# Kernel tuning notes

Measured on AMD Instinct MI355X. Metric: run time of the kernel, lower is better.

The kernel has to match this reference:

```python
import jax, jax.numpy as jnp
import numpy as np

PUPIL = 256          # pupil / OPD grid size
OUTPUT_DIM = 64      # cropped PSF postage-stamp size
N_BINS = 8           # number of SED wavelength bins
BATCH = 16
# Static, wavelength-dependent diffraction padding sizes (phase_N per bin).
# In the original these come from packed_SED_data[:,0,:] but are constant in a FoV.
PHASE_NS = [1024, 988, 952, 918, 886, 856, 828, 802]


def setup_inputs() -> dict:
    key = jax.random.key(0)
    k1, k2, k3 = jax.random.split(key, 3)
    # OPD in meters: small wavefront errors (~lambda/10 rms)
    opd_batch = jax.random.normal(k1, (BATCH, PUPIL, PUPIL), dtype=jnp.float32) * 1e-7
    # Annular pupil: outer aperture with central obscuration (like Euclid/VIS optics)
    yy, xx = np.mgrid[:PUPIL, :PUPIL].astype(np.float32)
    c = (PUPIL - 1) / 2.0
    r = np.sqrt((xx - c) ** 2 + (yy - c) ** 2) / (PUPIL / 2.0)
    obscurations = jnp.asarray(((r <= 1.0) & (r >= 0.3)).astype(np.float32))
    # Observed wavelengths per bin, in meters (visible band)
    lambdas = jnp.linspace(0.55e-6, 0.9e-6, N_BINS).astype(jnp.float32)
    # Normalized SED weights
    sed = jax.random.uniform(k2, (N_BINS,), dtype=jnp.float32) + 0.1
    sed_norms = sed / jnp.sum(sed)
    return {
        "opd_batch": opd_batch,
        "obscurations": obscurations,
        "lambdas": lambdas,
        "sed_norms": sed_norms,
    }


def _mono_psf(opd, obsc, lam, phase_N, out_dim):
    """Batched monochromatic PSF: OPD -> phase -> padded FFT -> cropped |.|^2, unit-sum."""
    # opd: [B, p, p]; phase = exp(i * 2pi/lambda * opd) * obscurations
    pre_phase = (2.0 * jnp.pi / lam) * opd
    phase = (jnp.cos(pre_phase) + 1j * jnp.sin(pre_phase)).astype(jnp.complex64)
    phase = phase * obsc.astype(jnp.complex64)
    p = opd.shape[-1]
    pad_lo = (phase_N - p) // 2
    pad_hi = phase_N - p - pad_lo
    padded = jnp.pad(phase, ((0, 0), (pad_lo, pad_hi), (pad_lo, pad_hi)))  # [B, N, N]
    fft = jnp.fft.fftshift(jnp.fft.fft2(padded), axes=(-2, -1))
    psf = fft.real ** 2 + fft.imag ** 2  # |FFT|^2, float32
    start = phase_N // 2 - out_dim // 2
    psf = psf[:, start:start + out_dim, start:start + out_dim]  # central crop
    return psf / jnp.sum(psf, axis=(-2, -1), keepdims=True)


def reference(opd_batch, obscurations, lambdas, sed_norms):
    # Polychromatic PSF: SED-weighted sum of monochromatic PSFs over wavelength bins.
    # Loop is over the small fixed set of bins (distinct static FFT sizes);
    # each bin is fully vectorized over the batch.
    out = jnp.zeros((opd_batch.shape[0], OUTPUT_DIM, OUTPUT_DIM), dtype=jnp.float32)
    for b, phase_N in enumerate(PHASE_NS):
        out = out + sed_norms[b] * _mono_psf(
            opd_batch, obscurations, lambdas[b], phase_N, OUTPUT_DIM
        )
    return out
```

## Files before the change

kernel.cpp:

```cpp
#include <hip/hip_runtime.h>
#include <math.h>

#define PUPIL 256
#define N_BINS 8
#define BATCH 16

__constant__ int PHASE_NS_C[N_BINS] = {1024, 988, 952, 918, 886, 856, 828, 802};

typedef short bf16x8 __attribute__((ext_vector_type(8)));
typedef short bf16x4 __attribute__((ext_vector_type(4)));
typedef float f32x4  __attribute__((ext_vector_type(4)));
typedef int   i32x4  __attribute__((ext_vector_type(4)));

#define MFMA16(a, b, c) __builtin_amdgcn_mfma_f32_16x16x32_bf16((a), (b), (c), 0, 0, 0)

__device__ __forceinline__ short f2bf(float f) {
  unsigned u = __float_as_uint(f);
  u += 0x7FFFu + ((u >> 16) & 1u);
  return (short)(u >> 16);
}
__device__ __forceinline__ bf16x8 neg8(bf16x8 v) {
  i32x4 t = __builtin_bit_cast(i32x4, v);
  t ^= (int)0x80008000;
  return __builtin_bit_cast(bf16x8, t);
}


__global__ void wprep(short* __restrict__ Wr_t, short* __restrict__ Wi_t) {
  int idx = blockIdx.x * 256 + threadIdx.x;
  int n   = idx & 255;
  int k   = (idx >> 8) & 63;
  int bin = idx >> 14;
  int N = PHASE_NS_C[bin];
  int m = ((k - 32) * n) % N;
  if (m < 0) m += N;
  float ang = -6.283185307179586f * (float)m / (float)N;
  float s, c;
  __sincosf(ang, &s, &c);
  Wr_t[idx] = f2bf(c);
  Wi_t[idx] = f2bf(s);
}

__global__ __launch_bounds__(256, 4) void stage1(
    const float* __restrict__ opd, const float* __restrict__ obsc,
    const float* __restrict__ lambdas,
    const short* __restrict__ Wr_t, const short* __restrict__ Wi_t,
    short* __restrict__ Gr_t, short* __restrict__ Gi_t)
{
  const int tid = threadIdx.x;
  const int yb = blockIdx.x * 32, bin = blockIdx.y, b = blockIdx.z;
  const int bb = b * N_BINS + bin;
  const float w0 = 6.283185307179586f / lambdas[bin];

  __shared__ short Pr[32 * 32], Pi[32 * 32];

  const int wave = tid >> 6, lane = tid & 63;
  const int lr = lane & 15, lq = lane >> 4;

  f32x4 aR[2], aI[2];
  aR[0] = (f32x4)0.0f; aR[1] = (f32x4)0.0f;
  aI[0] = (f32x4)0.0f; aI[1] = (f32x4)0.0f;

  const int gy = tid >> 3;
  const int gx = (tid & 7) * 4;
  const float* orow = opd + ((size_t)b * PUPIL + yb + gy) * PUPIL;
  const float* brow = obsc + (size_t)(yb + gy) * PUPIL;
  const short* wrb = Wr_t + ((size_t)bin * 64 + wave * 16 + lr) * 256 + lq * 8;
  const short* wib = Wi_t + ((size_t)bin * 64 + wave * 16 + lr) * 256 + lq * 8;

  for (int xc = 0; xc < 8; ++xc) {
    const int xb = xc * 32;
    const float4 od = *(const float4*)(orow + xb + gx);
    const float4 ob = *(const float4*)(brow + xb + gx);
    bf16x4 vr, vi;
    {
      float s, c;
      __sincosf(w0 * od.x, &s, &c); vr[0] = f2bf(c * ob.x); vi[0] = f2bf(s * ob.x);
      __sincosf(w0 * od.y, &s, &c); vr[1] = f2bf(c * ob.y); vi[1] = f2bf(s * ob.y);
      __sincosf(w0 * od.z, &s, &c); vr[2] = f2bf(c * ob.z); vi[2] = f2bf(s * ob.z);
      __sincosf(w0 * od.w, &s, &c); vr[3] = f2bf(c * ob.w); vi[3] = f2bf(s * ob.w);
    }
    __syncthreads();
    *(bf16x4*)&Pr[gy * 32 + gx] = vr;
    *(bf16x4*)&Pi[gy * 32 + gx] = vi;
    const bf16x8 w_r  = *(const bf16x8*)(wrb + xb);
    const bf16x8 w_i  = *(const bf16x8*)(wib + xb);
    const bf16x8 nw_i = neg8(w_i);
    __syncthreads();

    for (int t = 0; t < 2; ++t) {
      const bf16x8 pr = *(const bf16x8*)&Pr[(t * 16 + lr) * 32 + lq * 8];
      const bf16x8 pi = *(const bf16x8*)&Pi[(t * 16 + lr) * 32 + lq * 8];
      aR[t] = MFMA16(w_r,  pr, aR[t]);
      aR[t] = MFMA16(nw_i, pi, aR[t]);
      aI[t] = MFMA16(w_r,  pi, aI[t]);
      aI[t] = MFMA16(w_i,  pr, aI[t]);
    }
  }

  #pragma unroll
  for (int t = 0; t < 2; ++t) {
    const int y = yb + t * 16 + lr;
    #pragma unroll
    for (int r = 0; r < 4; ++r) {
      const int kv = wave * 16 + lq * 4 + r;
      const size_t o = ((size_t)bb * 64 + kv) * 256 + y;
      Gr_t[o] = f2bf(aR[t][r]);
      Gi_t[o] = f2bf(aI[t][r]);
    }
  }
}

__global__ __launch_bounds__(256, 4) void stage2(
    const short* __restrict__ Wr_t, const short* __restrict__ Wi_t,
    const short* __restrict__ Gr_t, const short* __restrict__ Gi_t,
    float* __restrict__ psf_raw, float* __restrict__ sums)
{
  const int tid = threadIdx.x;
  const int uc = blockIdx.x, bin = blockIdx.y, b = blockIdx.z;
  const int bb = b * N_BINS + bin;

  __shared__ float pvbuf[64 * 17];
  __shared__ float red[4];

  const int wave = tid >> 6, lane = tid & 63;
  const int lr = lane & 15, lq = lane >> 4;

  f32x4 hR = (f32x4)0.0f, hI = (f32x4)0.0f;

  const short* grb = Gr_t + ((size_t)bb * 64 + wave * 16 + lr) * 256 + lq * 8;
  const short* gib = Gi_t + ((size_t)bb * 64 + wave * 16 + lr) * 256 + lq * 8;
  const short* wrb = Wr_t + ((size_t)bin * 64 + uc * 16 + lr) * 256 + lq * 8;
  const short* wib = Wi_t + ((size_t)bin * 64 + uc * 16 + lr) * 256 + lq * 8;

  for (int yc = 0; yc < 8; ++yc) {
    const int yb = yc * 32;
    const bf16x8 g_r  = *(const bf16x8*)(grb + yb);
    const bf16x8 g_i  = *(const bf16x8*)(gib + yb);
    const bf16x8 w_r  = *(const bf16x8*)(wrb + yb);
    const bf16x8 w_i  = *(const bf16x8*)(wib + yb);
    const bf16x8 ng_i = neg8(g_i);
    hR = MFMA16(g_r,  w_r, hR);
    hR = MFMA16(ng_i, w_i, hR);
    hI = MFMA16(g_r,  w_i, hI);
    hI = MFMA16(g_i,  w_r, hI);
  }

  float pv[4], lsum = 0.f;
  #pragma unroll
  for (int r = 0; r < 4; ++r) {
    pv[r] = hR[r] * hR[r] + hI[r] * hI[r];
    lsum += pv[r];
  }
  #pragma unroll
  for (int off = 32; off > 0; off >>= 1) lsum += __shfl_down(lsum, off);
  if (lane == 0) red[wave] = lsum;

  #pragma unroll
  for (int r = 0; r < 4; ++r)
    pvbuf[(wave * 16 + lq * 4 + r) * 17 + lr] = pv[r];
  __syncthreads();

  if (tid == 0)
    sums[bb * 4 + uc] = red[0] + red[1] + red[2] + red[3];

  #pragma unroll
  for (int it = 0; it < 4; ++it) {
    const int i  = tid + it * 256;
    const int ul = i >> 6;
    const int v  = i & 63;
    psf_raw[(size_t)bb * 4096 + (uc * 16 + ul) * 64 + v] = pvbuf[v * 17 + ul];
  }
}

__global__ void combine(const float* __restrict__ psf_raw,
                        const float* __restrict__ sums,
                        const float* __restrict__ sed,
                        float* __restrict__ out) {
  __shared__ float sc[N_BINS];
  const int blk = blockIdx.x;
  const int b = blk >> 4;
  const int px = (blk & 15) * 256 + threadIdx.x;
  if (threadIdx.x < N_BINS) {
    const int bb = b * N_BINS + threadIdx.x;
    const float S = sums[bb * 4] + sums[bb * 4 + 1] + sums[bb * 4 + 2] + sums[bb * 4 + 3];
    sc[threadIdx.x] = sed[threadIdx.x] / S;
  }
  __syncthreads();
  float acc = 0.f;
  #pragma unroll
  for (int bin = 0; bin < N_BINS; ++bin)
    acc += sc[bin] * psf_raw[(size_t)(b * N_BINS + bin) * 4096 + px];
  out[b * 4096 + px] = acc;
}

extern "C" void kernel_launch(void* const* d_in, const int* in_sizes, int n_in,
                              void* d_out, int out_size, void* d_ws, size_t ws_size,
                              hipStream_t stream) {
  const float* opd     = (const float*)d_in[0];
  const float* obsc    = (const float*)d_in[1];
  const float* lambdas = (const float*)d_in[2];
  const float* sed     = (const float*)d_in[3];
  float* out = (float*)d_out;

  short* Wr_t = (short*)d_ws;
  short* Wi_t = Wr_t + (size_t)N_BINS * 64 * 256;
  short* Gr_t = Wi_t + (size_t)N_BINS * 64 * 256;
  short* Gi_t = Gr_t + (size_t)BATCH * N_BINS * 64 * 256;
  float* psf_raw = (float*)(Gi_t + (size_t)BATCH * N_BINS * 64 * 256);
  float* sums    = psf_raw + (size_t)BATCH * N_BINS * 4096;

  wprep<<<512, 256, 0, stream>>>(Wr_t, Wi_t);
  stage1<<<dim3(8, N_BINS, BATCH), 256, 0, stream>>>(opd, obsc, lambdas,
                                                     Wr_t, Wi_t, Gr_t, Gi_t);
  stage2<<<dim3(4, N_BINS, BATCH), 256, 0, stream>>>(Wr_t, Wi_t, Gr_t, Gi_t,
                                                     psf_raw, sums);
  combine<<<256, 256, 0, stream>>>(psf_raw, sums, sed, out);
}
```

Baseline: 88.18 us.

## Fuse twiddle prep into stage1 and combine into stage2 via atomics

Removes the separate twiddle-generation kernel by computing DFT twiddles inline in stage1 with sincos, with one block group per bin also writing them to workspace for stage2. Stage2 now computes the whole 64x64 output per (batch,bin) in one block, normalizes locally, and atomically accumulates SED-weighted results into the output, which stage1 zeroes first. This drops two kernel launches and the psf_raw round trip. In exchange it adds per-block sincos work, atomic float additions whose summation order is nondeterministic, and stage2 runs 4x fewer blocks.

```diff
diff --git a/kernel.cpp b/kernel.cpp
--- a/kernel.cpp
+++ b/kernel.cpp
@@ -26,36 +26,32 @@
 }
 
 
-__global__ void wprep(short* __restrict__ Wr_t, short* __restrict__ Wi_t) {
-  int idx = blockIdx.x * 256 + threadIdx.x;
-  int n   = idx & 255;
-  int k   = (idx >> 8) & 63;
-  int bin = idx >> 14;
-  int N = PHASE_NS_C[bin];
-  int m = ((k - 32) * n) % N;
-  if (m < 0) m += N;
-  float ang = -6.283185307179586f * (float)m / (float)N;
-  float s, c;
-  __sincosf(ang, &s, &c);
-  Wr_t[idx] = f2bf(c);
-  Wi_t[idx] = f2bf(s);
-}
-
 __global__ __launch_bounds__(256, 4) void stage1(
     const float* __restrict__ opd, const float* __restrict__ obsc,
     const float* __restrict__ lambdas,
-    const short* __restrict__ Wr_t, const short* __restrict__ Wi_t,
-    short* __restrict__ Gr_t, short* __restrict__ Gi_t)
+    short* __restrict__ Wr_t, short* __restrict__ Wi_t,
+    short* __restrict__ Gr_t, short* __restrict__ Gi_t,
+    float* __restrict__ out)
 {
   const int tid = threadIdx.x;
   const int yb = blockIdx.x * 32, bin = blockIdx.y, b = blockIdx.z;
   const int bb = b * N_BINS + bin;
   const float w0 = 6.283185307179586f / lambdas[bin];
+  const int   N  = PHASE_NS_C[bin];
+  const float npiN = -6.283185307179586f / (float)N;
+  const bool  storeW = (blockIdx.z == 0) && (blockIdx.x == 0);
 
   __shared__ short Pr[32 * 32], Pi[32 * 32];
+
+  if (tid < 64) {
+    const int blin = blockIdx.x + 8 * (blockIdx.y + 8 * blockIdx.z);
+    out[blin * 64 + tid] = 0.0f;
+  }
 
   const int wave = tid >> 6, lane = tid & 63;
   const int lr = lane & 15, lq = lane >> 4;
+  const int kv = wave * 16 + lr;
+  const int kvm = kv - 32;
 
   f32x4 aR[2], aI[2];
   aR[0] = (f32x4)0.0f; aR[1] = (f32x4)0.0f;
@@ -65,8 +61,6 @@
   const int gx = (tid & 7) * 4;
   const float* orow = opd + ((size_t)b * PUPIL + yb + gy) * PUPIL;
   const float* brow = obsc + (size_t)(yb + gy) * PUPIL;
-  const short* wrb = Wr_t + ((size_t)bin * 64 + wave * 16 + lr) * 256 + lq * 8;
-  const short* wib = Wi_t + ((size_t)bin * 64 + wave * 16 + lr) * 256 + lq * 8;
 
   for (int xc = 0; xc < 8; ++xc) {
     const int xb = xc * 32;
@@ -80,12 +74,25 @@
       __sincosf(w0 * od.z, &s, &c); vr[2] = f2bf(c * ob.z); vi[2] = f2bf(s * ob.z);
       __sincosf(w0 * od.w, &s, &c); vr[3] = f2bf(c * ob.w); vi[3] = f2bf(s * ob.w);
     }
+    bf16x8 w_r, w_i;
+    {
+      const int x0 = xb + lq * 8;
+      #pragma unroll
+      for (int j = 0; j < 8; ++j) {
+        float s, c;
+        __sincosf((float)(kvm * (x0 + j)) * npiN, &s, &c);
+        w_r[j] = f2bf(c);
+        w_i[j] = f2bf(s);
+      }
+    }
+    const bf16x8 nw_i = neg8(w_i);
+    if (storeW) {
+      *(bf16x8*)&Wr_t[((size_t)bin * 64 + kv) * 256 + xb + lq * 8] = w_r;
+      *(bf16x8*)&Wi_t[((size_t)bin * 64 + kv) * 256 + xb + lq * 8] = w_i;
+    }
     __syncthreads();
     *(bf16x4*)&Pr[gy * 32 + gx] = vr;
     *(bf16x4*)&Pi[gy * 32 + gx] = vi;
-    const bf16x8 w_r  = *(const bf16x8*)(wrb + xb);
-    const bf16x8 w_i  = *(const bf16x8*)(wib + xb);
-    const bf16x8 nw_i = neg8(w_i);
     __syncthreads();
 
     for (int t = 0; t < 2; ++t) {
@@ -103,95 +110,76 @@
     const int y = yb + t * 16 + lr;
     #pragma unroll
     for (int r = 0; r < 4; ++r) {
-      const int kv = wave * 16 + lq * 4 + r;
-      const size_t o = ((size_t)bb * 64 + kv) * 256 + y;
+      const int kvd = wave * 16 + lq * 4 + r;
+      const size_t o = ((size_t)bb * 64 + kvd) * 256 + y;
       Gr_t[o] = f2bf(aR[t][r]);
       Gi_t[o] = f2bf(aI[t][r]);
     }
   }
 }
 
-__global__ __launch_bounds__(256, 4) void stage2(
+__global__ __launch_bounds__(256, 2) void stage2(
     const short* __restrict__ Wr_t, const short* __restrict__ Wi_t,
     const short* __restrict__ Gr_t, const short* __restrict__ Gi_t,
-    float* __restrict__ psf_raw, float* __restrict__ sums)
+    const float* __restrict__ sed, float* __restrict__ out)
 {
   const int tid = threadIdx.x;
-  const int uc = blockIdx.x, bin = blockIdx.y, b = blockIdx.z;
+  const int bin = blockIdx.x, b = blockIdx.y;
   const int bb = b * N_BINS + bin;
 
-  __shared__ float pvbuf[64 * 17];
   __shared__ float red[4];
 
   const int wave = tid >> 6, lane = tid & 63;
   const int lr = lane & 15, lq = lane >> 4;
 
-  f32x4 hR = (f32x4)0.0f, hI = (f32x4)0.0f;
+  f32x4 hR[4], hI[4];
+  #pragma unroll
+  for (int n = 0; n < 4; ++n) { hR[n] = (f32x4)0.0f; hI[n] = (f32x4)0.0f; }
 
   const short* grb = Gr_t + ((size_t)bb * 64 + wave * 16 + lr) * 256 + lq * 8;
   const short* gib = Gi_t + ((size_t)bb * 64 + wave * 16 + lr) * 256 + lq * 8;
-  const short* wrb = Wr_t + ((size_t)bin * 64 + uc * 16 + lr) * 256 + lq * 8;
-  const short* wib = Wi_t + ((size_t)bin * 64 + uc * 16 + lr) * 256 + lq * 8;
+  const size_t wbase = ((size_t)bin * 64 + lr) * 256 + lq * 8;
 
   for (int yc = 0; yc < 8; ++yc) {
     const int yb = yc * 32;
     const bf16x8 g_r  = *(const bf16x8*)(grb + yb);
     const bf16x8 g_i  = *(const bf16x8*)(gib + yb);
-    const bf16x8 w_r  = *(const bf16x8*)(wrb + yb);
-    const bf16x8 w_i  = *(const bf16x8*)(wib + yb);
     const bf16x8 ng_i = neg8(g_i);
-    hR = MFMA16(g_r,  w_r, hR);
-    hR = MFMA16(ng_i, w_i, hR);
-    hI = MFMA16(g_r,  w_i, hI);
-    hI = MFMA16(g_i,  w_r, hI);
-  }
-
-  float pv[4], lsum = 0.f;
-  #pragma unroll
-  for (int r = 0; r < 4; ++r) {
-    pv[r] = hR[r] * hR[r] + hI[r] * hI[r];
-    lsum += pv[r];
-  }
+    for (int n = 0; n < 4; ++n) {
+      const bf16x8 w_r = *(const bf16x8*)(Wr_t + wbase + (size_t)n * 16 * 256 + yb);
+      const bf16x8 w_i = *(const bf16x8*)(Wi_t + wbase + (size_t)n * 16 * 256 + yb);
+      hR[n] = MFMA16(g_r,  w_r, hR[n]);
+      hR[n] = MFMA16(ng_i, w_i, hR[n]);
+      hI[n] = MFMA16(g_r,  w_i, hI[n]);
+      hI[n] = MFMA16(g_i,  w_r, hI[n]);
+    }
+  }
+
+  float pv[4][4], lsum = 0.f;
+  #pragma unroll
+  for (int n = 0; n < 4; ++n)
+    #pragma unroll
+    for (int r = 0; r < 4; ++r) {
+      pv[n][r] = hR[n][r] * hR[n][r] + hI[n][r] * hI[n][r];
+      lsum += pv[n][r];
+    }
   #pragma unroll
   for (int off = 32; off > 0; off >>= 1) lsum += __shfl_down(lsum, off);
   if (lane == 0) red[wave] = lsum;
-
-  #pragma unroll
-  for (int r = 0; r < 4; ++r)
-    pvbuf[(wave * 16 + lq * 4 + r) * 17 + lr] = pv[r];
   __syncthreads();
-
-  if (tid == 0)
-    sums[bb * 4 + uc] = red[0] + red[1] + red[2] + red[3];
-
-  #pragma unroll
-  for (int it = 0; it < 4; ++it) {
-    const int i  = tid + it * 256;
-    const int ul = i >> 6;
-    const int v  = i & 63;
-    psf_raw[(size_t)bb * 4096 + (uc * 16 + ul) * 64 + v] = pvbuf[v * 17 + ul];
-  }
-}
-
-__global__ void combine(const float* __restrict__ psf_raw,
-                        const float* __restrict__ sums,
-                        const float* __restrict__ sed,
-                        float* __restrict__ out) {
-  __shared__ float sc[N_BINS];
-  const int blk = blockIdx.x;
-  const int b = blk >> 4;
-  const int px = (blk & 15) * 256 + threadIdx.x;
-  if (threadIdx.x < N_BINS) {
-    const int bb = b * N_BINS + threadIdx.x;
-    const float S = sums[bb * 4] + sums[bb * 4 + 1] + sums[bb * 4 + 2] + sums[bb * 4 + 3];
-    sc[threadIdx.x] = sed[threadIdx.x] / S;
-  }
-  __syncthreads();
-  float acc = 0.f;
-  #pragma unroll
-  for (int bin = 0; bin < N_BINS; ++bin)
-    acc += sc[bin] * psf_raw[(size_t)(b * N_BINS + bin) * 4096 + px];
-  out[b * 4096 + px] = acc;
+  const float S = red[0] + red[1] + red[2] + red[3];
+  const float scale = sed[bin] / S;
+
+  float* ob = out + (size_t)b * 4096;
+  #pragma unroll
+  for (int n = 0; n < 4; ++n) {
+    const int u = n * 16 + lr;
+    #pragma unroll
+    for (int r = 0; r < 4; ++r) {
+      const int v = wave * 16 + lq * 4 + r;
+      atomicAdd(&ob[u * 64 + v], pv[n][r] * scale);
+    }
+  }
 }
 
 extern "C" void kernel_launch(void* const* d_in, const int* in_sizes, int n_in,
@@ -207,13 +195,9 @@
   short* Wi_t = Wr_t + (size_t)N_BINS * 64 * 256;
   short* Gr_t = Wi_t + (size_t)N_BINS * 64 * 256;
   short* Gi_t = Gr_t + (size_t)BATCH * N_BINS * 64 * 256;
-  float* psf_raw = (float*)(Gi_t + (size_t)BATCH * N_BINS * 64 * 256);
-  float* sums    = psf_raw + (size_t)BATCH * N_BINS * 4096;
-
-  wprep<<<512, 256, 0, stream>>>(Wr_t, Wi_t);
+
   stage1<<<dim3(8, N_BINS, BATCH), 256, 0, stream>>>(opd, obsc, lambdas,
-                                                     Wr_t, Wi_t, Gr_t, Gi_t);
-  stage2<<<dim3(4, N_BINS, BATCH), 256, 0, stream>>>(Wr_t, Wi_t, Gr_t, Gi_t,
-                                                     psf_raw, sums);
-  combine<<<256, 256, 0, stream>>>(psf_raw, sums, sed, out);
-}
+                                                     Wr_t, Wi_t, Gr_t, Gi_t, out);
+  stage2<<<dim3(N_BINS, BATCH), 256, 0, stream>>>(Wr_t, Wi_t, Gr_t, Gi_t,
+                                                  sed, out);
+}
```

New measurement: 97.22 us. +10.2%, slower.

## Fuse all stages into one cooperative kernel with grid syncs and in-register twiddles

Applied to the files above, without the earlier changes.

Merges the twiddle-prep, both DFT matmul stages and the SED combine into a single cooperative kernel of 256 blocks of 512 threads, separated by grid-wide syncs. This removes three kernel launches and the gaps between them. Stage-1 twiddles are now generated in registers by angle-recurrence rotation instead of being loaded from global memory. Blocks with b==0 and yc==0 also write the twiddles out for stage 2 to read. The trade-offs are grid-sync overhead, the need for every block to be co-resident, and some bf16 accuracy drift from the recurrence.

```diff
diff --git a/kernel.cpp b/kernel.cpp
--- a/kernel.cpp
+++ b/kernel.cpp
@@ -1,5 +1,8 @@
 #include <hip/hip_runtime.h>
+#include <hip/hip_cooperative_groups.h>
 #include <math.h>
+
+namespace cg = cooperative_groups;
 
 #define PUPIL 256
 #define N_BINS 8
@@ -26,172 +29,182 @@
 }
 
 
-__global__ void wprep(short* __restrict__ Wr_t, short* __restrict__ Wi_t) {
-  int idx = blockIdx.x * 256 + threadIdx.x;
-  int n   = idx & 255;
-  int k   = (idx >> 8) & 63;
-  int bin = idx >> 14;
-  int N = PHASE_NS_C[bin];
-  int m = ((k - 32) * n) % N;
-  if (m < 0) m += N;
-  float ang = -6.283185307179586f * (float)m / (float)N;
-  float s, c;
-  __sincosf(ang, &s, &c);
-  Wr_t[idx] = f2bf(c);
-  Wi_t[idx] = f2bf(s);
-}
-
-__global__ __launch_bounds__(256, 4) void stage1(
+__global__ __launch_bounds__(512, 2) void mega(
     const float* __restrict__ opd, const float* __restrict__ obsc,
-    const float* __restrict__ lambdas,
-    const short* __restrict__ Wr_t, const short* __restrict__ Wi_t,
-    short* __restrict__ Gr_t, short* __restrict__ Gi_t)
+    const float* __restrict__ lambdas, const float* __restrict__ sed,
+    short* __restrict__ Wr_t, short* __restrict__ Wi_t,
+    short* __restrict__ Gr_t, short* __restrict__ Gi_t,
+    float* __restrict__ psf_raw, float* __restrict__ sums,
+    float* __restrict__ out)
 {
+  const int blk = blockIdx.x;
   const int tid = threadIdx.x;
-  const int yb = blockIdx.x * 32, bin = blockIdx.y, b = blockIdx.z;
-  const int bb = b * N_BINS + bin;
-  const float w0 = 6.283185307179586f / lambdas[bin];
-
-  __shared__ short Pr[32 * 32], Pi[32 * 32];
-
-  const int wave = tid >> 6, lane = tid & 63;
+  const int h    = tid >> 8;
+  const int htid = tid & 255;
+
+  __shared__ short Pr[2][32 * 32], Pi[2][32 * 32];
+  __shared__ float pvbuf[2][64 * 17];
+  __shared__ float red[2][4];
+  __shared__ float sc[N_BINS];
+
+  const int wave = htid >> 6, lane = htid & 63;
   const int lr = lane & 15, lq = lane >> 4;
 
-  f32x4 aR[2], aI[2];
-  aR[0] = (f32x4)0.0f; aR[1] = (f32x4)0.0f;
-  aI[0] = (f32x4)0.0f; aI[1] = (f32x4)0.0f;
-
-  const int gy = tid >> 3;
-  const int gx = (tid & 7) * 4;
-  const float* orow = opd + ((size_t)b * PUPIL + yb + gy) * PUPIL;
-  const float* brow = obsc + (size_t)(yb + gy) * PUPIL;
-  const short* wrb = Wr_t + ((size_t)bin * 64 + wave * 16 + lr) * 256 + lq * 8;
-  const short* wib = Wi_t + ((size_t)bin * 64 + wave * 16 + lr) * 256 + lq * 8;
-
-  for (int xc = 0; xc < 8; ++xc) {
-    const int xb = xc * 32;
-    const float4 od = *(const float4*)(orow + xb + gx);
-    const float4 ob = *(const float4*)(brow + xb + gx);
-    bf16x4 vr, vi;
-    {
-      float s, c;
-      __sincosf(w0 * od.x, &s, &c); vr[0] = f2bf(c * ob.x); vi[0] = f2bf(s * ob.x);
-      __sincosf(w0 * od.y, &s, &c); vr[1] = f2bf(c * ob.y); vi[1] = f2bf(s * ob.y);
-      __sincosf(w0 * od.z, &s, &c); vr[2] = f2bf(c * ob.z); vi[2] = f2bf(s * ob.z);
-      __sincosf(w0 * od.w, &s, &c); vr[3] = f2bf(c * ob.w); vi[3] = f2bf(s * ob.w);
-    }
+  for (int it = 0; it < 2; ++it) {
+    const int unit = (blk * 2 + h) * 2 + it;
+    const int yc = unit & 7, bin = (unit >> 3) & 7, b = unit >> 6;
+    const int yb = yc * 32;
+    const int bb = b * N_BINS + bin;
+    const float w0 = 6.283185307179586f / lambdas[bin];
+    const float npiN = -6.283185307179586f / (float)PHASE_NS_C[bin];
+    const bool storeW = (yc == 0) && (b == 0);
+
+    const int kvm = wave * 16 + lr - 32;
+    float stepS, stepC;
+    __sincosf((float)kvm * npiN, &stepS, &stepC);
+
+    f32x4 aR[2], aI[2];
+    aR[0] = (f32x4)0.0f; aR[1] = (f32x4)0.0f;
+    aI[0] = (f32x4)0.0f; aI[1] = (f32x4)0.0f;
+
+    const int gy = htid >> 3;
+    const int gx = (htid & 7) * 4;
+    const float* orow = opd + ((size_t)b * PUPIL + yb + gy) * PUPIL;
+    const float* brow = obsc + (size_t)(yb + gy) * PUPIL;
+
+    for (int xc = 0; xc < 8; ++xc) {
+      const int xb = xc * 32;
+      const float4 od = *(const float4*)(orow + xb + gx);
+      const float4 ob = *(const float4*)(brow + xb + gx);
+      bf16x4 vr, vi;
+      {
+        float s, c;
+        __sincosf(w0 * od.x, &s, &c); vr[0] = f2bf(c * ob.x); vi[0] = f2bf(s * ob.x);
+        __sincosf(w0 * od.y, &s, &c); vr[1] = f2bf(c * ob.y); vi[1] = f2bf(s * ob.y);
+        __sincosf(w0 * od.z, &s, &c); vr[2] = f2bf(c * ob.z); vi[2] = f2bf(s * ob.z);
+        __sincosf(w0 * od.w, &s, &c); vr[3] = f2bf(c * ob.w); vi[3] = f2bf(s * ob.w);
+      }
+      bf16x8 w_r, w_i;
+      {
+        const int x0 = xb + lq * 8;
+        float ps, pc;
+        __sincosf((float)(kvm * x0) * npiN, &ps, &pc);
+        w_r[0] = f2bf(pc); w_i[0] = f2bf(ps);
+        #pragma unroll
+        for (int j = 1; j < 8; ++j) {
+          const float nc = pc * stepC - ps * stepS;
+          const float ns = pc * stepS + ps * stepC;
+          w_r[j] = f2bf(nc); w_i[j] = f2bf(ns);
+          pc = nc; ps = ns;
+        }
+      }
+      const bf16x8 nw_i = neg8(w_i);
+      if (storeW) {
+        const int kv = wave * 16 + lr;
+        *(bf16x8*)&Wr_t[((size_t)bin * 64 + kv) * 256 + xb + lq * 8] = w_r;
+        *(bf16x8*)&Wi_t[((size_t)bin * 64 + kv) * 256 + xb + lq * 8] = w_i;
+      }
+      __syncthreads();
+      *(bf16x4*)&Pr[h][gy * 32 + gx] = vr;
+      *(bf16x4*)&Pi[h][gy * 32 + gx] = vi;
+      __syncthreads();
+
+      for (int t = 0; t < 2; ++t) {
+        const bf16x8 pr = *(const bf16x8*)&Pr[h][(t * 16 + lr) * 32 + lq * 8];
+        const bf16x8 pi = *(const bf16x8*)&Pi[h][(t * 16 + lr) * 32 + lq * 8];
+        aR[t] = MFMA16(w_r,  pr, aR[t]);
+        aR[t] = MFMA16(nw_i, pi, aR[t]);
+        aI[t] = MFMA16(w_r,  pi, aI[t]);
+        aI[t] = MFMA16(w_i,  pr, aI[t]);
+      }
+    }
+
+    #pragma unroll
+    for (int t = 0; t < 2; ++t) {
+      const int y = yb + t * 16 + lr;
+      #pragma unroll
+      for (int r = 0; r < 4; ++r) {
+        const int kvd = wave * 16 + lq * 4 + r;
+        const size_t o = ((size_t)bb * 64 + kvd) * 256 + y;
+        Gr_t[o] = f2bf(aR[t][r]);
+        Gi_t[o] = f2bf(aI[t][r]);
+      }
+    }
+  }
+
+  cg::this_grid().sync();
+
+  {
+    const int unit = blk * 2 + h;
+    const int uc = unit & 3, bin = (unit >> 2) & 7, b = unit >> 5;
+    const int bb = b * N_BINS + bin;
+
+    f32x4 hR = (f32x4)0.0f, hI = (f32x4)0.0f;
+
+    const short* grb = Gr_t + ((size_t)bb * 64 + wave * 16 + lr) * 256 + lq * 8;
+    const short* gib = Gi_t + ((size_t)bb * 64 + wave * 16 + lr) * 256 + lq * 8;
+    const short* wrb = Wr_t + ((size_t)bin * 64 + uc * 16 + lr) * 256 + lq * 8;
+    const short* wib = Wi_t + ((size_t)bin * 64 + uc * 16 + lr) * 256 + lq * 8;
+
+    for (int yc2 = 0; yc2 < 8; ++yc2) {
+      const int yb2 = yc2 * 32;
+      const bf16x8 g_r  = *(const bf16x8*)(grb + yb2);
+      const bf16x8 g_i  = *(const bf16x8*)(gib + yb2);
+      const bf16x8 w_r  = *(const bf16x8*)(wrb + yb2);
+      const bf16x8 w_i  = *(const bf16x8*)(wib + yb2);
+      const bf16x8 ng_i = neg8(g_i);
+      hR = MFMA16(g_r,  w_r, hR);
+      hR = MFMA16(ng_i, w_i, hR);
+      hI = MFMA16(g_r,  w_i, hI);
+      hI = MFMA16(g_i,  w_r, hI);
+    }
+
+    float pv[4], lsum = 0.f;
+    #pragma unroll
+    for (int r = 0; r < 4; ++r) {
+      pv[r] = hR[r] * hR[r] + hI[r] * hI[r];
+      lsum += pv[r];
+    }
+    #pragma unroll
+    for (int off = 32; off > 0; off >>= 1) lsum += __shfl_down(lsum, off);
+    if (lane == 0) red[h][wave] = lsum;
+
+    #pragma unroll
+    for (int r = 0; r < 4; ++r)
+      pvbuf[h][(wave * 16 + lq * 4 + r) * 17 + lr] = pv[r];
     __syncthreads();
-    *(bf16x4*)&Pr[gy * 32 + gx] = vr;
-    *(bf16x4*)&Pi[gy * 32 + gx] = vi;
-    const bf16x8 w_r  = *(const bf16x8*)(wrb + xb);
-    const bf16x8 w_i  = *(const bf16x8*)(wib + xb);
-    const bf16x8 nw_i = neg8(w_i);
+
+    if (htid == 0)
+      sums[bb * 4 + uc] = red[h][0] + red[h][1] + red[h][2] + red[h][3];
+
+    #pragma unroll
+    for (int it = 0; it < 4; ++it) {
+      const int i  = htid + it * 256;
+      const int ul = i >> 6;
+      const int v  = i & 63;
+      psf_raw[(size_t)bb * 4096 + (uc * 16 + ul) * 64 + v] = pvbuf[h][v * 17 + ul];
+    }
+  }
+
+  cg::this_grid().sync();
+
+  {
+    const int b = blk >> 4;
+    if (tid < N_BINS) {
+      const int bb = b * N_BINS + tid;
+      const float S = sums[bb * 4] + sums[bb * 4 + 1] + sums[bb * 4 + 2] + sums[bb * 4 + 3];
+      sc[tid] = sed[tid] / S;
+    }
     __syncthreads();
-
-    for (int t = 0; t < 2; ++t) {
-      const bf16x8 pr = *(const bf16x8*)&Pr[(t * 16 + lr) * 32 + lq * 8];
-      const bf16x8 pi = *(const bf16x8*)&Pi[(t * 16 + lr) * 32 + lq * 8];
-      aR[t] = MFMA16(w_r,  pr, aR[t]);
-      aR[t] = MFMA16(nw_i, pi, aR[t]);
-      aI[t] = MFMA16(w_r,  pi, aI[t]);
-      aI[t] = MFMA16(w_i,  pr, aI[t]);
+    if (tid < 256) {
+      const int px = (blk & 15) * 256 + tid;
+      float acc = 0.f;
+      #pragma unroll
+      for (int bin = 0; bin < N_BINS; ++bin)
+        acc += sc[bin] * psf_raw[(size_t)(b * N_BINS + bin) * 4096 + px];
+      out[b * 4096 + px] = acc;
     }
   }
-
-  #pragma unroll
-  for (int t = 0; t < 2; ++t) {
-    const int y = yb + t * 16 + lr;
-    #pragma unroll
-    for (int r = 0; r < 4; ++r) {
-      const int kv = wave * 16 + lq * 4 + r;
-      const size_t o = ((size_t)bb * 64 + kv) * 256 + y;
-      Gr_t[o] = f2bf(aR[t][r]);
-      Gi_t[o] = f2bf(aI[t][r]);
-    }
-  }
-}
-
-__global__ __launch_bounds__(256, 4) void stage2(
-    const short* __restrict__ Wr_t, const short* __restrict__ Wi_t,
-    const short* __restrict__ Gr_t, const short* __restrict__ Gi_t,
-    float* __restrict__ psf_raw, float* __restrict__ sums)
-{
-  const int tid = threadIdx.x;
-  const int uc = blockIdx.x, bin = blockIdx.y, b = blockIdx.z;
-  const int bb = b * N_BINS + bin;
-
-  __shared__ float pvbuf[64 * 17];
-  __shared__ float red[4];
-
-  const int wave = tid >> 6, lane = tid & 63;
-  const int lr = lane & 15, lq = lane >> 4;
-
-  f32x4 hR = (f32x4)0.0f, hI = (f32x4)0.0f;
-
-  const short* grb = Gr_t + ((size_t)bb * 64 + wave * 16 + lr) * 256 + lq * 8;
-  const short* gib = Gi_t + ((size_t)bb * 64 + wave * 16 + lr) * 256 + lq * 8;
-  const short* wrb = Wr_t + ((size_t)bin * 64 + uc * 16 + lr) * 256 + lq * 8;
-  const short* wib = Wi_t + ((size_t)bin * 64 + uc * 16 + lr) * 256 + lq * 8;
-
-  for (int yc = 0; yc < 8; ++yc) {
-    const int yb = yc * 32;
-    const bf16x8 g_r  = *(const bf16x8*)(grb + yb);
-    const bf16x8 g_i  = *(const bf16x8*)(gib + yb);
-    const bf16x8 w_r  = *(const bf16x8*)(wrb + yb);
-    const bf16x8 w_i  = *(const bf16x8*)(wib + yb);
-    const bf16x8 ng_i = neg8(g_i);
-    hR = MFMA16(g_r,  w_r, hR);
-    hR = MFMA16(ng_i, w_i, hR);
-    hI = MFMA16(g_r,  w_i, hI);
-    hI = MFMA16(g_i,  w_r, hI);
-  }
-
-  float pv[4], lsum = 0.f;
-  #pragma unroll
-  for (int r = 0; r < 4; ++r) {
-    pv[r] = hR[r] * hR[r] + hI[r] * hI[r];
-    lsum += pv[r];
-  }
-  #pragma unroll
-  for (int off = 32; off > 0; off >>= 1) lsum += __shfl_down(lsum, off);
-  if (lane == 0) red[wave] = lsum;
-
-  #pragma unroll
-  for (int r = 0; r < 4; ++r)
-    pvbuf[(wave * 16 + lq * 4 + r) * 17 + lr] = pv[r];
-  __syncthreads();
-
-  if (tid == 0)
-    sums[bb * 4 + uc] = red[0] + red[1] + red[2] + red[3];
-
-  #pragma unroll
-  for (int it = 0; it < 4; ++it) {
-    const int i  = tid + it * 256;
-    const int ul = i >> 6;
-    const int v  = i & 63;
-    psf_raw[(size_t)bb * 4096 + (uc * 16 + ul) * 64 + v] = pvbuf[v * 17 + ul];
-  }
-}
-
-__global__ void combine(const float* __restrict__ psf_raw,
-                        const float* __restrict__ sums,
-                        const float* __restrict__ sed,
-                        float* __restrict__ out) {
-  __shared__ float sc[N_BINS];
-  const int blk = blockIdx.x;
-  const int b = blk >> 4;
-  const int px = (blk & 15) * 256 + threadIdx.x;
-  if (threadIdx.x < N_BINS) {
-    const int bb = b * N_BINS + threadIdx.x;
-    const float S = sums[bb * 4] + sums[bb * 4 + 1] + sums[bb * 4 + 2] + sums[bb * 4 + 3];
-    sc[threadIdx.x] = sed[threadIdx.x] / S;
-  }
-  __syncthreads();
-  float acc = 0.f;
-  #pragma unroll
-  for (int bin = 0; bin < N_BINS; ++bin)
-    acc += sc[bin] * psf_raw[(size_t)(b * N_BINS + bin) * 4096 + px];
-  out[b * 4096 + px] = acc;
 }
 
 extern "C" void kernel_launch(void* const* d_in, const int* in_sizes, int n_in,
@@ -210,10 +223,8 @@
   float* psf_raw = (float*)(Gi_t + (size_t)BATCH * N_BINS * 64 * 256);
   float* sums    = psf_raw + (size_t)BATCH * N_BINS * 4096;
 
-  wprep<<<512, 256, 0, stream>>>(Wr_t, Wi_t);
-  stage1<<<dim3(8, N_BINS, BATCH), 256, 0, stream>>>(opd, obsc, lambdas,
-                                                     Wr_t, Wi_t, Gr_t, Gi_t);
-  stage2<<<dim3(4, N_BINS, BATCH), 256, 0, stream>>>(Wr_t, Wi_t, Gr_t, Gi_t,
-                                                     psf_raw, sums);
-  combine<<<256, 256, 0, stream>>>(psf_raw, sums, sed, out);
-}
+  void* args[] = {(void*)&opd, (void*)&obsc, (void*)&lambdas, (void*)&sed,
+                  (void*)&Wr_t, (void*)&Wi_t, (void*)&Gr_t, (void*)&Gi_t,
+                  (void*)&psf_raw, (void*)&sums, (void*)&out};
+  hipLaunchCooperativeKernel((void*)mega, dim3(256), dim3(512), args, 0, stream);
+}
```

Measured after the change: 166.7 us. 1.89x slower.

## Compute pupil phase directly in MFMA registers and prefetch stage2 operands

Applied to the files above, without the earlier changes.

Stage1 now has each wave own 16 pupil rows and compute the bf16 phase values directly in the B-operand register layout. This removes the shared-memory staging and both __syncthreads per chunk. Each block covers 64 rows and all 64 output frequencies, so the grid is halved, each thread holds four accumulator tiles, and launch bounds are relaxed to 2 blocks per CU. Stage2 software-prefetches the next chunk's G and W operands before issuing the current MFMAs, to hide load latency. The cost is more register pressure and fewer blocks in stage1, and every wave now loads all four W tiles itself.

```diff
diff --git a/kernel.cpp b/kernel.cpp
--- a/kernel.cpp
+++ b/kernel.cpp
@@ -8,7 +8,6 @@
 __constant__ int PHASE_NS_C[N_BINS] = {1024, 988, 952, 918, 886, 856, 828, 802};
 
 typedef short bf16x8 __attribute__((ext_vector_type(8)));
-typedef short bf16x4 __attribute__((ext_vector_type(4)));
 typedef float f32x4  __attribute__((ext_vector_type(4)));
 typedef int   i32x4  __attribute__((ext_vector_type(4)));
 
@@ -41,56 +40,52 @@
   Wi_t[idx] = f2bf(s);
 }
 
-__global__ __launch_bounds__(256, 4) void stage1(
+__global__ __launch_bounds__(256, 2) void stage1(
     const float* __restrict__ opd, const float* __restrict__ obsc,
     const float* __restrict__ lambdas,
     const short* __restrict__ Wr_t, const short* __restrict__ Wi_t,
     short* __restrict__ Gr_t, short* __restrict__ Gi_t)
 {
   const int tid = threadIdx.x;
-  const int yb = blockIdx.x * 32, bin = blockIdx.y, b = blockIdx.z;
+  const int yb = blockIdx.x * 64, bin = blockIdx.y, b = blockIdx.z;
   const int bb = b * N_BINS + bin;
   const float w0 = 6.283185307179586f / lambdas[bin];
 
-  __shared__ short Pr[32 * 32], Pi[32 * 32];
-
   const int wave = tid >> 6, lane = tid & 63;
   const int lr = lane & 15, lq = lane >> 4;
 
-  f32x4 aR[2], aI[2];
-  aR[0] = (f32x4)0.0f; aR[1] = (f32x4)0.0f;
-  aI[0] = (f32x4)0.0f; aI[1] = (f32x4)0.0f;
-
-  const int gy = tid >> 3;
-  const int gx = (tid & 7) * 4;
-  const float* orow = opd + ((size_t)b * PUPIL + yb + gy) * PUPIL;
-  const float* brow = obsc + (size_t)(yb + gy) * PUPIL;
-  const short* wrb = Wr_t + ((size_t)bin * 64 + wave * 16 + lr) * 256 + lq * 8;
-  const short* wib = Wi_t + ((size_t)bin * 64 + wave * 16 + lr) * 256 + lq * 8;
+  const int y  = yb + wave * 16 + lr;
+  const int x0 = lq * 8;
+
+  const float* orow = opd + ((size_t)b * PUPIL + y) * PUPIL;
+  const float* brow = obsc + (size_t)y * PUPIL;
+  const short* wrb = Wr_t + ((size_t)bin * 64 + lr) * 256 + x0;
+  const short* wib = Wi_t + ((size_t)bin * 64 + lr) * 256 + x0;
+
+  f32x4 aR[4], aI[4];
+  #pragma unroll
+  for (int t = 0; t < 4; ++t) { aR[t] = (f32x4)0.0f; aI[t] = (f32x4)0.0f; }
 
   for (int xc = 0; xc < 8; ++xc) {
     const int xb = xc * 32;
-    const float4 od = *(const float4*)(orow + xb + gx);
-    const float4 ob = *(const float4*)(brow + xb + gx);
-    bf16x4 vr, vi;
-    {
+    float od[8], ob[8];
+    *(float4*)&od[0] = *(const float4*)(orow + xb + x0);
+    *(float4*)&od[4] = *(const float4*)(orow + xb + x0 + 4);
+    *(float4*)&ob[0] = *(const float4*)(brow + xb + x0);
+    *(float4*)&ob[4] = *(const float4*)(brow + xb + x0 + 4);
+    bf16x8 pr, pi;
+    #pragma unroll
+    for (int j = 0; j < 8; ++j) {
       float s, c;
-      __sincosf(w0 * od.x, &s, &c); vr[0] = f2bf(c * ob.x); vi[0] = f2bf(s * ob.x);
-      __sincosf(w0 * od.y, &s, &c); vr[1] = f2bf(c * ob.y); vi[1] = f2bf(s * ob.y);
-      __sincosf(w0 * od.z, &s, &c); vr[2] = f2bf(c * ob.z); vi[2] = f2bf(s * ob.z);
-      __sincosf(w0 * od.w, &s, &c); vr[3] = f2bf(c * ob.w); vi[3] = f2bf(s * ob.w);
-    }
-    __syncthreads();
-    *(bf16x4*)&Pr[gy * 32 + gx] = vr;
-    *(bf16x4*)&Pi[gy * 32 + gx] = vi;
-    const bf16x8 w_r  = *(const bf16x8*)(wrb + xb);
-    const bf16x8 w_i  = *(const bf16x8*)(wib + xb);
-    const bf16x8 nw_i = neg8(w_i);
-    __syncthreads();
-
-    for (int t = 0; t < 2; ++t) {
-      const bf16x8 pr = *(const bf16x8*)&Pr[(t * 16 + lr) * 32 + lq * 8];
-      const bf16x8 pi = *(const bf16x8*)&Pi[(t * 16 + lr) * 32 + lq * 8];
+      __sincosf(w0 * od[j], &s, &c);
+      pr[j] = f2bf(c * ob[j]);
+      pi[j] = f2bf(s * ob[j]);
+    }
+    #pragma unroll
+    for (int t = 0; t < 4; ++t) {
+      const bf16x8 w_r  = *(const bf16x8*)(wrb + (size_t)t * 16 * 256 + xb);
+      const bf16x8 w_i  = *(const bf16x8*)(wib + (size_t)t * 16 * 256 + xb);
+      const bf16x8 nw_i = neg8(w_i);
       aR[t] = MFMA16(w_r,  pr, aR[t]);
       aR[t] = MFMA16(nw_i, pi, aR[t]);
       aI[t] = MFMA16(w_r,  pi, aI[t]);
@@ -99,16 +94,14 @@
   }
 
   #pragma unroll
-  for (int t = 0; t < 2; ++t) {
-    const int y = yb + t * 16 + lr;
+  for (int t = 0; t < 4; ++t)
     #pragma unroll
     for (int r = 0; r < 4; ++r) {
-      const int kv = wave * 16 + lq * 4 + r;
+      const int kv = t * 16 + lq * 4 + r;
       const size_t o = ((size_t)bb * 64 + kv) * 256 + y;
       Gr_t[o] = f2bf(aR[t][r]);
       Gi_t[o] = f2bf(aI[t][r]);
     }
-  }
 }
 
 __global__ __launch_bounds__(256, 4) void stage2(
@@ -133,17 +126,25 @@
   const short* wrb = Wr_t + ((size_t)bin * 64 + uc * 16 + lr) * 256 + lq * 8;
   const short* wib = Wi_t + ((size_t)bin * 64 + uc * 16 + lr) * 256 + lq * 8;
 
+  bf16x8 g_r = *(const bf16x8*)(grb);
+  bf16x8 g_i = *(const bf16x8*)(gib);
+  bf16x8 w_r = *(const bf16x8*)(wrb);
+  bf16x8 w_i = *(const bf16x8*)(wib);
+
   for (int yc = 0; yc < 8; ++yc) {
-    const int yb = yc * 32;
-    const bf16x8 g_r  = *(const bf16x8*)(grb + yb);
-    const bf16x8 g_i  = *(const bf16x8*)(gib + yb);
-    const bf16x8 w_r  = *(const bf16x8*)(wrb + yb);
-    const bf16x8 w_i  = *(const bf16x8*)(wib + yb);
-    const bf16x8 ng_i = neg8(g_i);
-    hR = MFMA16(g_r,  w_r, hR);
-    hR = MFMA16(ng_i, w_i, hR);
-    hI = MFMA16(g_r,  w_i, hI);
-    hI = MFMA16(g_i,  w_r, hI);
+    const bf16x8 cg_r = g_r, cg_i = g_i, cw_r = w_r, cw_i = w_i;
+    if (yc < 7) {
+      const int yn = (yc + 1) * 32;
+      g_r = *(const bf16x8*)(grb + yn);
+      g_i = *(const bf16x8*)(gib + yn);
+      w_r = *(const bf16x8*)(wrb + yn);
+      w_i = *(const bf16x8*)(wib + yn);
+    }
+    const bf16x8 ng_i = neg8(cg_i);
+    hR = MFMA16(cg_r, cw_r, hR);
+    hR = MFMA16(ng_i, cw_i, hR);
+    hI = MFMA16(cg_r, cw_i, hI);
+    hI = MFMA16(cg_i, cw_r, hI);
   }
 
   float pv[4], lsum = 0.f;
@@ -211,7 +212,7 @@
   float* sums    = psf_raw + (size_t)BATCH * N_BINS * 4096;
 
   wprep<<<512, 256, 0, stream>>>(Wr_t, Wi_t);
-  stage1<<<dim3(8, N_BINS, BATCH), 256, 0, stream>>>(opd, obsc, lambdas,
+  stage1<<<dim3(4, N_BINS, BATCH), 256, 0, stream>>>(opd, obsc, lambdas,
                                                      Wr_t, Wi_t, Gr_t, Gi_t);
   stage2<<<dim3(4, N_BINS, BATCH), 256, 0, stream>>>(Wr_t, Wi_t, Gr_t, Gi_t,
                                                      psf_raw, sums);
```

Result: slower. 102.1 us (+15.8%).
